# Kernel optimization log

Measured on AMD Instinct MI355X. Metric: run time of the kernel, lower is better.

## Reference

```python
import jax, jax.numpy as jnp
import numpy as np

B, G = 256, 24
N = B * G
D_IN, HEADS, D_HEAD = 128, 8, 64  # out_channels = in_channels//2 = 64, concat=False
EFF = HEADS * D_HEAD
EPS = 1e-5
SCALE = float(np.sqrt(D_HEAD))

def _gelu(x):
    return jax.nn.gelu(x, approximate=False)

def _pff(x, w1, b1, w2, b2):
    # PositionwiseFeedForward, dropout=0 (eval)
    return _gelu(x @ w1.T + b1) @ w2.T + b2

def _graph_norm_global(x, w, b, ms):
    # GraphNorm called without batch -> single graph over all N nodes
    mean = jnp.mean(x, axis=0, keepdims=True)
    out = x - mean * ms
    var = jnp.mean(out * out, axis=0, keepdims=True)
    return w * out / jnp.sqrt(var + EPS) + b

def _graph_norm(x, w, b, ms, batch, nseg):
    cnt = jax.ops.segment_sum(jnp.ones((x.shape[0],), x.dtype), batch, nseg)[:, None]
    mean = jax.ops.segment_sum(x, batch, nseg) / cnt
    out = x - mean[batch] * ms
    var = jax.ops.segment_sum(out * out, batch, nseg) / cnt
    return w * out / jnp.sqrt(var + EPS)[batch] + b

def _segment_softmax(logits, seg, nseg):
    m = jax.ops.segment_max(logits, seg, num_segments=nseg)
    e = jnp.exp(logits - m[seg])
    s = jax.ops.segment_sum(e, seg, num_segments=nseg)
    return e / (s[seg] + 1e-16)

def _attn_conv(x, edge_index, p):
    (nq_w, nq_b, nq_ms, wq, bq, wk, bk, wv, bv,
     no_w, no_b, no_ms, o_w1, o_b1, o_w2, o_b2) = p
    n = x.shape[0]
    xin = x
    xn = _graph_norm_global(x, nq_w, nq_b, nq_ms)
    q = (xn @ wq.T + bq).reshape(n, HEADS, D_HEAD)
    k = (xn @ wk.T + bk).reshape(n, HEADS, D_HEAD)
    v = (xn @ wv.T + bv).reshape(n, HEADS, D_HEAD)
    loops = jnp.arange(n, dtype=edge_index.dtype)  # add_self_loops appends
    src = jnp.concatenate([edge_index[0], loops])
    dst = jnp.concatenate([edge_index[1], loops])
    qk = jnp.sum(q[dst] * k[src], axis=-1) / SCALE          # [E', H]
    alpha = _segment_softmax(qk, dst, n)                     # segment softmax over dst
    aggr = jax.ops.segment_sum(v[src] * alpha[:, :, None], dst, num_segments=n)  # [N,H,Dh]
    aggr = aggr.mean(axis=1)                                 # concat=False: head mean -> [N,64]
    init = xin.reshape(n, D_IN // D_HEAD, D_HEAD).sum(axis=1)  # sum-fold 128 -> 64 residual
    h = aggr + init
    hn = _graph_norm_global(h, no_w, no_b, no_ms)
    return h + _pff(hn, o_w1, o_b1, o_w2, o_b2)


def setup_inputs() -> dict:
    key = jax.random.key(0)
    ks = jax.random.split(key, 12)
    # block-dense edges: fully connected within each set, no self loops
    a = np.arange(G)
    ii, jj = np.meshgrid(a, a, indexing='ij')
    m = ii != jj
    dst_l, src_l = ii[m], jj[m]
    offs = (np.arange(B) * G)[:, None]
    src = (src_l[None, :] + offs).reshape(-1)
    dst = (dst_l[None, :] + offs).reshape(-1)
    edge_index = jnp.asarray(np.stack([src, dst]), dtype=jnp.int64)
    batch = jnp.asarray(np.repeat(np.arange(B), G), dtype=jnp.int64)
    ptr = jnp.asarray(np.arange(B + 1) * G, dtype=jnp.int64)
    x = jax.random.normal(ks[0], (N, D_IN), jnp.float32)
    def lin(k, o, i):
        return jax.random.normal(k, (o, i), jnp.float32) * (1.0 / np.sqrt(i))
    d = dict(x=x, edge_index=edge_index, ptr=ptr, batch=batch)
    d.update(nq_w=jnp.ones((D_IN,)), nq_b=jnp.zeros((D_IN,)), nq_ms=jnp.ones((D_IN,)))
    d.update(wq=lin(ks[1], EFF, D_IN), bq=jnp.zeros((EFF,)),
             wk=lin(ks[2], EFF, D_IN), bk=jnp.zeros((EFF,)),
             wv=lin(ks[3], EFF, D_IN), bv=jnp.zeros((EFF,)))
    d.update(no_w=jnp.ones((D_HEAD,)), no_b=jnp.zeros((D_HEAD,)), no_ms=jnp.ones((D_HEAD,)))
    d.update(o_w1=lin(ks[4], D_HEAD, D_HEAD), o_b1=jnp.zeros((D_HEAD,)),
             o_w2=lin(ks[5], D_HEAD, D_HEAD), o_b2=jnp.zeros((D_HEAD,)))
    d.update(pn_w=jnp.ones((D_HEAD,)), pn_b=jnp.zeros((D_HEAD,)), pn_ms=jnp.ones((D_HEAD,)))
    d.update(p_w1=lin(ks[6], D_HEAD, D_HEAD), p_b1=jnp.zeros((D_HEAD,)),
             p_w2=lin(ks[7], 1, D_HEAD), p_b2=jnp.zeros((1,)))
    return d


def reference(x, edge_index, ptr, batch,
              nq_w, nq_b, nq_ms, wq, bq, wk, bk, wv, bv,
              no_w, no_b, no_ms, o_w1, o_b1, o_w2, o_b2,
              pn_w, pn_b, pn_ms, p_w1, p_b1, p_w2, p_b2):
    nseg = ptr.shape[0] - 1
    h = _attn_conv(x, edge_index,
                   (nq_w, nq_b, nq_ms, wq, bq, wk, bk, wv, bv,
                    no_w, no_b, no_ms, o_w1, o_b1, o_w2, o_b2))   # [N,64]
    hn = _graph_norm(h, pn_w, pn_b, pn_ms, batch, nseg)
    score = _pff(hn, p_w1, p_b1, p_w2, p_b2)                       # [N,1]
    w = _segment_softmax(score[:, 0], batch, nseg)[:, None]        # per-set softmax
    return jax.ops.segment_sum(x * w, batch, num_segments=nseg)    # [B, 128]
```

## Files before the change

### kernel.cpp

```cpp
#include <hip/hip_runtime.h>
#include <stdint.h>


#define N_NODES 6144
#define GSIZE 24
#define NGRAPH 256
#define DIN 128
#define DH 64
#define EFF 512
#define EPSN 1e-5f

typedef __attribute__((ext_vector_type(8))) __bf16 bf16x8;
typedef __attribute__((ext_vector_type(4))) float f32x4;
union U16B { uint4 u; bf16x8 v; unsigned short s[8]; };

__device__ inline float bf2f(unsigned short u){ return __uint_as_float(((unsigned)u)<<16); }
__device__ inline unsigned short f2bf(float f){
  unsigned u = __float_as_uint(f);
  u += 0x7fff + ((u>>16)&1);
  return (unsigned short)(u>>16);
}
__device__ inline float gelu_exact(float x){ return 0.5f*x*(1.0f+erff(x*0.70710678118654752f)); }

#define XP    0
#define HP    49152
#define WT1   81920
#define WT2   86016
#define PWT1  90112
#define FBo   94208
#define AC    94720
#define AC2   94976
#define WCVT_BYTE  385024
#define HCOMB_BYTE 778240
#define QKV_BYTE   2359296

__global__ __launch_bounds__(256)
void k_pre(const float* __restrict__ x,
           const float* __restrict__ o_w1, const float* __restrict__ o_w2,
           const float* __restrict__ p_w1,
           const float* __restrict__ o_b1, const float* __restrict__ o_b2,
           const float* __restrict__ p_b1, const float* __restrict__ p_w2,
           const float* __restrict__ p_b2,
           const float* __restrict__ wq, const float* __restrict__ wk,
           const float* __restrict__ wv,
           float* __restrict__ wsf){
  int t = threadIdx.x;
  int bi = blockIdx.x;
  if(bi < 192){
    int c = t & 127, h = t >> 7;
    float s = 0.f, q = 0.f;
    #pragma unroll
    for(int r = 0; r < 16; ++r){
      float v = x[(size_t)(bi*32 + h + 2*r)*DIN + c];
      s += v; q += v*v;
    }
    __shared__ float sm[256], sm2[256];
    sm[t] = s; sm2[t] = q;
    __syncthreads();
    if(t < 128){
      wsf[XP + bi*256 + t]       = sm[t] + sm[t+128];
      wsf[XP + bi*256 + 128 + t] = sm2[t] + sm2[t+128];
    }
    return;
  }
  if(bi < 195){
    const float* src; float* dst;
    if(bi == 192){ src = o_w1; dst = wsf + WT1; }
    else if(bi == 193){ src = o_w2; dst = wsf + WT2; }
    else { src = p_w1; dst = wsf + PWT1; }
    for(int p = t; p < DH*DH; p += 256){
      int r = p >> 6, c = p & 63;
      dst[c*DH + r] = src[p];
    }
    if(bi == 192){
      float* fb = wsf + FBo;
      if(t < 64){
        fb[t]       = o_b1[t];
        fb[64 + t]  = o_b2[t];
        fb[128 + t] = p_b1[t];
        fb[192 + t] = p_w2[t];
      }
      if(t == 0) fb[256] = p_b2[0];
    }
    return;
  }
  int j = bi - 195;
  int mat = j >> 2, seg = j & 3;
  const float* src = (mat==0) ? wq : (mat==1) ? wk : wv;
  unsigned short* dst = (unsigned short*)((char*)wsf + WCVT_BYTE)
                        + (size_t)mat*EFF*DIN + seg*16384;
  const float* sp = src + seg*16384;
  for(int e = t*8; e < 16384; e += 2048){
    float4 a = *(const float4*)(sp + e);
    float4 b = *(const float4*)(sp + e + 4);
    U16B o;
    o.s[0]=f2bf(a.x); o.s[1]=f2bf(a.y); o.s[2]=f2bf(a.z); o.s[3]=f2bf(a.w);
    o.s[4]=f2bf(b.x); o.s[5]=f2bf(b.y); o.s[6]=f2bf(b.z); o.s[7]=f2bf(b.w);
    *(uint4*)(dst + e) = o.u;
  }
}

__global__ __launch_bounds__(512)
void k_stats(const float* __restrict__ nq_w, const float* __restrict__ nq_b,
             const float* __restrict__ nq_ms, float* __restrict__ ws){
  __shared__ float redA[512], redB[512];
  int t = threadIdx.x;
  int c = t & 127, grp = t >> 7;
  float s = 0.f, q = 0.f;
  for(int p = grp*48; p < grp*48 + 48; ++p){
    s += ws[XP + p*256 + c];
    q += ws[XP + p*256 + 128 + c];
  }
  redA[t] = s; redB[t] = q;
  __syncthreads();
  if(t < 128){
    float s1 = redA[t] + redA[t+128] + redA[t+256] + redA[t+384];
    float q1 = redB[t] + redB[t+128] + redB[t+256] + redB[t+384];
    float mean = s1 * (1.0f / N_NODES);
    float ex2  = q1 * (1.0f / N_NODES);
    float cm   = mean * nq_ms[t];
    float var  = ex2 - 2.f*cm*mean + cm*cm;
    float rstd = rsqrtf(var + EPSN);
    float a    = nq_w[t] * rstd;
    ws[AC + t]       = a;
    ws[AC + 128 + t] = nq_b[t] - a*cm;
  }
}

__global__ __launch_bounds__(256)
void k_qkv(const float* __restrict__ x,
           const float* __restrict__ bq, const float* __restrict__ bk,
           const float* __restrict__ bv,
           const float* __restrict__ ws, float* __restrict__ qkv){
  __shared__ __align__(16) char lds[65536];
  char* Alds = lds;
  char* Blds = lds + 32768;
  int t = threadIdx.x;
  int mt = blockIdx.x / 12, nt = blockIdx.x % 12;
  int mat = nt >> 2, obase = (nt & 3) * 128;
  const float* A1c = ws + AC;
  const unsigned short* wsrc = (const unsigned short*)((const char*)ws + WCVT_BYTE)
                               + (size_t)mat*EFF*DIN + (size_t)obase*DIN;
  {
    int kf = (t & 31) * 4;
    float4 a4 = *(const float4*)(A1c + kf);
    float4 c4 = *(const float4*)(A1c + 128 + kf);
    #pragma unroll
    for(int it = 0; it < 16; ++it){
      int row = it*8 + (t >> 5);
      float4 v = *(const float4*)(x + (size_t)(mt*128 + row)*DIN + kf);
      ushort4 us;
      us.x = f2bf(v.x*a4.x + c4.x);
      us.y = f2bf(v.y*a4.y + c4.y);
      us.z = f2bf(v.z*a4.z + c4.z);
      us.w = f2bf(v.w*a4.w + c4.w);
      *(ushort4*)(Alds + ((row*256 + kf*2) ^ ((row & 7) << 4))) = us;
    }
  }
  {
    int kb = (t & 15) * 16;
    #pragma unroll
    for(int it = 0; it < 8; ++it){
      int row = it*16 + (t >> 4);
      uint4 w = *(const uint4*)((const char*)wsrc + row*256 + kb);
      *(uint4*)(Blds + ((row*256 + kb) ^ ((row & 7) << 4))) = w;
    }
  }
  __syncthreads();
  int wv4 = t >> 6, l = t & 63;
  int wr = wv4 >> 1, wc = wv4 & 1;
  int lm = l & 15, lq = l >> 4;
  f32x4 acc[4][4];
  #pragma unroll
  for(int m = 0; m < 4; ++m)
    #pragma unroll
    for(int n = 0; n < 4; ++n) acc[m][n] = (f32x4){0.f,0.f,0.f,0.f};
  #pragma unroll
  for(int kk = 0; kk < 4; ++kk){
    int kbyte = kk*64 + lq*16;
    bf16x8 af[4], bf[4];
    #pragma unroll
    for(int m = 0; m < 4; ++m){
      int row = wr*64 + m*16 + lm;
      af[m] = *(const bf16x8*)(Alds + ((row*256 + kbyte) ^ ((row & 7) << 4)));
    }
    #pragma unroll
    for(int n = 0; n < 4; ++n){
      int row = wc*64 + n*16 + lm;
      bf[n] = *(const bf16x8*)(Blds + ((row*256 + kbyte) ^ ((row & 7) << 4)));
    }
    #pragma unroll
    for(int m = 0; m < 4; ++m)
      #pragma unroll
      for(int n = 0; n < 4; ++n)
        acc[m][n] = __builtin_amdgcn_mfma_f32_16x16x32_bf16(af[m], bf[n], acc[m][n], 0, 0, 0);
  }
  const float* bias = (mat==0) ? bq : (mat==1) ? bk : bv;
  #pragma unroll
  for(int n = 0; n < 4; ++n){
    float bn = bias[obase + wc*64 + n*16 + lm];
    int gcol = nt*128 + wc*64 + n*16 + lm;
    #pragma unroll
    for(int m = 0; m < 4; ++m){
      int grow0 = mt*128 + wr*64 + m*16 + lq*4;
      #pragma unroll
      for(int r = 0; r < 4; ++r)
        qkv[(size_t)(grow0 + r)*1536 + gcol] = acc[m][n][r] + bn;
    }
  }
}

__global__ __launch_bounds__(512)
void k_attn(const float* __restrict__ x, const float* __restrict__ qkv,
            float* __restrict__ ws, float* __restrict__ hcomb){
  __shared__ __align__(16) float ST[8][GSIZE][28];
  __shared__ __align__(16) float hv[GSIZE][68];
  int t = threadIdx.x, g = blockIdx.x, base = g * GSIZE;
  int h = t >> 6, l = t & 63;

  for(int i = t; i < GSIZE*68; i += 512) ((float*)hv)[i] = 0.f;

  int r0 = 3*(l >> 3), j0 = 3*(l & 7);
  const float* qp = qkv + (size_t)(base + r0)*1536 + h*64;
  const float* kp = qkv + (size_t)(base + j0)*1536 + 512 + h*64;
  float s00=0.f,s01=0.f,s02=0.f,s10=0.f,s11=0.f,s12=0.f,s20=0.f,s21=0.f,s22=0.f;
  #pragma unroll
  for(int d4 = 0; d4 < 16; ++d4){
    float4 q0 = *(const float4*)(qp + d4*4);
    float4 q1 = *(const float4*)(qp + 1536 + d4*4);
    float4 q2 = *(const float4*)(qp + 3072 + d4*4);
    float4 k0 = *(const float4*)(kp + d4*4);
    float4 k1 = *(const float4*)(kp + 1536 + d4*4);
    float4 k2 = *(const float4*)(kp + 3072 + d4*4);
    s00 += q0.x*k0.x + q0.y*k0.y + q0.z*k0.z + q0.w*k0.w;
    s01 += q0.x*k1.x + q0.y*k1.y + q0.z*k1.z + q0.w*k1.w;
    s02 += q0.x*k2.x + q0.y*k2.y + q0.z*k2.z + q0.w*k2.w;
    s10 += q1.x*k0.x + q1.y*k0.y + q1.z*k0.z + q1.w*k0.w;
    s11 += q1.x*k1.x + q1.y*k1.y + q1.z*k1.z + q1.w*k1.w;
    s12 += q1.x*k2.x + q1.y*k2.y + q1.z*k2.z + q1.w*k2.w;
    s20 += q2.x*k0.x + q2.y*k0.y + q2.z*k0.z + q2.w*k0.w;
    s21 += q2.x*k1.x + q2.y*k1.y + q2.z*k1.z + q2.w*k1.w;
    s22 += q2.x*k2.x + q2.y*k2.y + q2.z*k2.z + q2.w*k2.w;
  }
  {
    float a0, a1, a2, m0, su, inv;
    a0 = s00*0.125f; a1 = s01*0.125f; a2 = s02*0.125f;
    m0 = fmaxf(fmaxf(a0, a1), a2);
    #pragma unroll
    for(int o = 1; o < 8; o <<= 1) m0 = fmaxf(m0, __shfl_xor(m0, o, 8));
    a0 = __expf(a0-m0); a1 = __expf(a1-m0); a2 = __expf(a2-m0);
    su = a0 + a1 + a2;
    #pragma unroll
    for(int o = 1; o < 8; o <<= 1) su += __shfl_xor(su, o, 8);
    inv = 1.0f/(su + 1e-16f);
    ST[h][j0+0][r0+0] = a0*inv; ST[h][j0+1][r0+0] = a1*inv; ST[h][j0+2][r0+0] = a2*inv;
    a0 = s10*0.125f; a1 = s11*0.125f; a2 = s12*0.125f;
    m0 = fmaxf(fmaxf(a0, a1), a2);
    #pragma unroll
    for(int o = 1; o < 8; o <<= 1) m0 = fmaxf(m0, __shfl_xor(m0, o, 8));
    a0 = __expf(a0-m0); a1 = __expf(a1-m0); a2 = __expf(a2-m0);
    su = a0 + a1 + a2;
    #pragma unroll
    for(int o = 1; o < 8; o <<= 1) su += __shfl_xor(su, o, 8);
    inv = 1.0f/(su + 1e-16f);
    ST[h][j0+0][r0+1] = a0*inv; ST[h][j0+1][r0+1] = a1*inv; ST[h][j0+2][r0+1] = a2*inv;
    a0 = s20*0.125f; a1 = s21*0.125f; a2 = s22*0.125f;
    m0 = fmaxf(fmaxf(a0, a1), a2);
    #pragma unroll
    for(int o = 1; o < 8; o <<= 1) m0 = fmaxf(m0, __shfl_xor(m0, o, 8));
    a0 = __expf(a0-m0); a1 = __expf(a1-m0); a2 = __expf(a2-m0);
    su = a0 + a1 + a2;
    #pragma unroll
    for(int o = 1; o < 8; o <<= 1) su += __shfl_xor(su, o, 8);
    inv = 1.0f/(su + 1e-16f);
    ST[h][j0+0][r0+2] = a0*inv; ST[h][j0+1][r0+2] = a1*inv; ST[h][j0+2][r0+2] = a2*inv;
  }
  __syncthreads();

  {
    float o24[GSIZE];
    #pragma unroll
    for(int r = 0; r < GSIZE; ++r) o24[r] = 0.f;
    const float* vp = qkv + (size_t)base*1536 + 1024 + h*64 + l;
    #pragma unroll
    for(int j = 0; j < GSIZE; ++j){
      float v = vp[(size_t)j*1536];
      #pragma unroll
      for(int rq = 0; rq < 6; ++rq){
        float4 p4 = *(const float4*)&ST[h][j][rq*4];
        o24[rq*4+0] = fmaf(p4.x, v, o24[rq*4+0]);
        o24[rq*4+1] = fmaf(p4.y, v, o24[rq*4+1]);
        o24[rq*4+2] = fmaf(p4.z, v, o24[rq*4+2]);
        o24[rq*4+3] = fmaf(p4.w, v, o24[rq*4+3]);
      }
    }
    #pragma unroll
    for(int r = 0; r < GSIZE; ++r) atomicAdd(&hv[r][l], o24[r]);
  }
  __syncthreads();

  #pragma unroll
  for(int sl = 0; sl < 3; ++sl){
    int idx = t + sl*512;
    int r = idx >> 6, d = idx & 63;
    const float* xr = x + (size_t)(base + r)*DIN;
    float hval = hv[r][d]*0.125f + xr[d] + xr[64 + d];
    hcomb[(size_t)(base + r)*DH + d] = hval;
    hv[r][d] = hval;
  }
  __syncthreads();
  if(t < 64){
    float s1 = 0.f, s2 = 0.f;
    #pragma unroll
    for(int i = 0; i < GSIZE; ++i){ float v = hv[i][t]; s1 += v; s2 += v*v; }
    ws[HP + g*128 + t]      = s1;
    ws[HP + g*128 + 64 + t] = s2;
  }
}

__global__ __launch_bounds__(256)
void k_hstats(const float* __restrict__ no_w, const float* __restrict__ no_b,
              const float* __restrict__ no_ms, float* __restrict__ ws){
  __shared__ float redA[256], redB[256];
  int t = threadIdx.x;
  int c = t & 63, grp = t >> 6;
  float s1 = 0.f, s2 = 0.f;
  for(int p = grp; p < NGRAPH; p += 4){
    s1 += ws[HP + p*128 + c];
    s2 += ws[HP + p*128 + 64 + c];
  }
  redA[t] = s1; redB[t] = s2;
  __syncthreads();
  if(t < DH){
    float a1 = redA[t] + redA[t+64] + redA[t+128] + redA[t+192];
    float a2 = redB[t] + redB[t+64] + redB[t+128] + redB[t+192];
    float mean = a1 * (1.0f / N_NODES);
    float ex2  = a2 * (1.0f / N_NODES);
    float cm   = mean * no_ms[t];
    float var  = ex2 - 2.f*cm*mean + cm*cm;
    float rstd = rsqrtf(var + EPSN);
    float a    = no_w[t] * rstd;
    ws[AC2 + t]      = a;
    ws[AC2 + 64 + t] = no_b[t] - a*cm;
  }
}

__global__ __launch_bounds__(256)
void k_final(const float* __restrict__ x,
             const float* __restrict__ hbuf, const float* __restrict__ ws,
             const float* __restrict__ pn_w, const float* __restrict__ pn_b,
             const float* __restrict__ pn_ms,
             float* __restrict__ out){
  __shared__ __align__(16) float W1[4096];
  __shared__ __align__(16) float W2[4096];
  __shared__ __align__(16) float PW1[4096];
  __shared__ __align__(16) float fbs[260];
  __shared__ __align__(16) float hs[GSIZE][68];
  __shared__ __align__(16) float hn[GSIZE][68];
  __shared__ __align__(16) float ts[GSIZE][68];
  __shared__ float a3[DH], c3[DH];
  __shared__ float scores[GSIZE], wsm[GSIZE];

  int t = threadIdx.x;
  int base = blockIdx.x * GSIZE;
  int c = t & 63, i0 = t >> 6;

  {
    const float4* s1 = (const float4*)(ws + WT1);
    const float4* s2 = (const float4*)(ws + WT2);
    const float4* s3 = (const float4*)(ws + PWT1);
    #pragma unroll
    for(int it = 0; it < 4; ++it){
      int i = t + it*256;
      ((float4*)W1)[i]  = s1[i];
      ((float4*)W2)[i]  = s2[i];
      ((float4*)PW1)[i] = s3[i];
    }
    if(t < 257) fbs[t] = ws[FBo + t];
  }
  {
    float a2 = ws[AC2 + c];
    float c2 = ws[AC2 + 64 + c];
    #pragma unroll
    for(int r = 0; r < 6; ++r){
      int i = i0 + 4*r;
      float hvv = hbuf[(size_t)(base + i)*DH + c];
      hs[i][c] = hvv;
      hn[i][c] = a2*hvv + c2;
    }
  }
  __syncthreads();

  {
    float acc[6];
    #pragma unroll
    for(int r = 0; r < 6; ++r) acc[r] = fbs[c];
    #pragma unroll 16
    for(int k = 0; k < DH; ++k){
      float w = W1[k*DH + c];
      #pragma unroll
      for(int r = 0; r < 6; ++r) acc[r] = fmaf(hn[i0 + 4*r][k], w, acc[r]);
    }
    #pragma unroll
    for(int r = 0; r < 6; ++r) ts[i0 + 4*r][c] = gelu_exact(acc[r]);
  }
  __syncthreads();

  {
    float acc[6];
    #pragma unroll
    for(int r = 0; r < 6; ++r) acc[r] = fbs[64 + c];
    #pragma unroll 16
    for(int k = 0; k < DH; ++k){
      float w = W2[k*DH + c];
      #pragma unroll
      for(int r = 0; r < 6; ++r) acc[r] = fmaf(ts[i0 + 4*r][k], w, acc[r]);
    }
    #pragma unroll
    for(int r = 0; r < 6; ++r) hs[i0 + 4*r][c] += acc[r];
  }
  __syncthreads();

  if(t < DH){
    float s1 = 0.f, s2 = 0.f;
    #pragma unroll
    for(int i = 0; i < GSIZE; i++){ float v = hs[i][t]; s1 += v; s2 += v*v; }
    float mean = s1 * (1.0f / GSIZE);
    float ex2  = s2 * (1.0f / GSIZE);
    float cm   = mean * pn_ms[t];
    float var  = ex2 - 2.f*cm*mean + cm*cm;
    float rstd = rsqrtf(var + EPSN);
    float a    = pn_w[t] * rstd;
    a3[t] = a; c3[t] = pn_b[t] - a*cm;
  }
  __syncthreads();

  {
    float acc[6];
    #pragma unroll
    for(int r = 0; r < 6; ++r) acc[r] = fbs[128 + c];
    #pragma unroll 16
    for(int k = 0; k < DH; ++k){
      float w  = PW1[k*DH + c];
      float ak = a3[k], ck = c3[k];
      #pragma unroll
      for(int r = 0; r < 6; ++r){
        float hnv = fmaf(ak, hs[i0 + 4*r][k], ck);
        acc[r] = fmaf(hnv, w, acc[r]);
      }
    }
    #pragma unroll
    for(int r = 0; r < 6; ++r) ts[i0 + 4*r][c] = gelu_exact(acc[r]);
  }
  __syncthreads();

  if(t < GSIZE){
    const float4* tp = (const float4*)ts[t];
    const float4* wp = (const float4*)(fbs + 192);
    float s = fbs[256];
    #pragma unroll
    for(int q = 0; q < 16; ++q){
      float4 a = tp[q], b = wp[q];
      s += a.x*b.x + a.y*b.y + a.z*b.z + a.w*b.w;
    }
    scores[t] = s;
  }
  __syncthreads();
  if(t < GSIZE){
    float mx = -1e30f;
    #pragma unroll
    for(int j = 0; j < GSIZE; j++) mx = fmaxf(mx, scores[j]);
    float sum = 0.f;
    #pragma unroll
    for(int j = 0; j < GSIZE; j++) sum += __expf(scores[j] - mx);
    wsm[t] = __expf(scores[t] - mx) / (sum + 1e-16f);
  }
  __syncthreads();
  if(t < DIN){
    float s = 0.f;
    #pragma unroll 8
    for(int i = 0; i < GSIZE; i++) s += wsm[i] * x[(size_t)(base+i)*DIN + t];
    out[(size_t)blockIdx.x*DIN + t] = s;
  }
}

extern "C" void kernel_launch(void* const* d_in, const int* in_sizes, int n_in,
                              void* d_out, int out_size, void* d_ws, size_t ws_size,
                              hipStream_t stream){
  (void)in_sizes; (void)n_in; (void)out_size; (void)ws_size;
  const float* x    = (const float*)d_in[0];
  const float* nq_w = (const float*)d_in[4];
  const float* nq_b = (const float*)d_in[5];
  const float* nq_ms= (const float*)d_in[6];
  const float* wq   = (const float*)d_in[7];
  const float* bq   = (const float*)d_in[8];
  const float* wk   = (const float*)d_in[9];
  const float* bk   = (const float*)d_in[10];
  const float* wv   = (const float*)d_in[11];
  const float* bv   = (const float*)d_in[12];
  const float* no_w = (const float*)d_in[13];
  const float* no_b = (const float*)d_in[14];
  const float* no_ms= (const float*)d_in[15];
  const float* o_w1 = (const float*)d_in[16];
  const float* o_b1 = (const float*)d_in[17];
  const float* o_w2 = (const float*)d_in[18];
  const float* o_b2 = (const float*)d_in[19];
  const float* pn_w = (const float*)d_in[20];
  const float* pn_b = (const float*)d_in[21];
  const float* pn_ms= (const float*)d_in[22];
  const float* p_w1 = (const float*)d_in[23];
  const float* p_b1 = (const float*)d_in[24];
  const float* p_w2 = (const float*)d_in[25];
  const float* p_b2 = (const float*)d_in[26];

  float* ws    = (float*)d_ws;
  float* hcomb = (float*)((char*)d_ws + HCOMB_BYTE);
  float* qkvb  = (float*)((char*)d_ws + QKV_BYTE);

  k_pre<<<207, 256, 0, stream>>>(x, o_w1, o_w2, p_w1, o_b1, o_b2, p_b1, p_w2, p_b2,
                                 wq, wk, wv, ws);
  k_stats<<<1, 512, 0, stream>>>(nq_w, nq_b, nq_ms, ws);
  k_qkv<<<576, 256, 0, stream>>>(x, bq, bk, bv, ws, qkvb);
  k_attn<<<NGRAPH, 512, 0, stream>>>(x, qkvb, ws, hcomb);
  k_hstats<<<1, 256, 0, stream>>>(no_w, no_b, no_ms, ws);
  k_final<<<NGRAPH, 256, 0, stream>>>(x, hcomb, ws, pn_w, pn_b, pn_ms, (float*)d_out);
}
```

Measured before the change: 195.6 us.

## Fuse global stats, QKV projection and attention into one per-graph kernel

The single-block stats kernels are folded into the consumers: every attention block recomputes the global norm stats, and k_final recomputes the output-norm stats. The QKV GEMM now runs per graph inside the attention kernel, with results kept in LDS instead of a global qkv buffer. This cuts three kernel launches and the round trip of a large intermediate through global memory. In exchange, each block redundantly reduces the global partial sums and uses a large LDS footprint (about 150KB), which lowers occupancy. MFMA tiles are also partly wasted because 24 rows are padded to 32.

```diff
diff --git a/kernel.cpp b/kernel.cpp
--- a/kernel.cpp
+++ b/kernel.cpp
@@ -14,7 +14,6 @@
 typedef __attribute__((ext_vector_type(4))) float f32x4;
 union U16B { uint4 u; bf16x8 v; unsigned short s[8]; };
 
-__device__ inline float bf2f(unsigned short u){ return __uint_as_float(((unsigned)u)<<16); }
 __device__ inline unsigned short f2bf(float f){
   unsigned u = __float_as_uint(f);
   u += 0x7fff + ((u>>16)&1);
@@ -28,11 +27,10 @@
 #define WT2   86016
 #define PWT1  90112
 #define FBo   94208
-#define AC    94720
-#define AC2   94976
 #define WCVT_BYTE  385024
 #define HCOMB_BYTE 778240
-#define QKV_BYTE   2359296
+
+#define QSTRIDE 516
 
 __global__ __launch_bounds__(256)
 void k_pre(const float* __restrict__ x,
@@ -101,149 +99,123 @@
 }
 
 __global__ __launch_bounds__(512)
-void k_stats(const float* __restrict__ nq_w, const float* __restrict__ nq_b,
-             const float* __restrict__ nq_ms, float* __restrict__ ws){
-  __shared__ float redA[512], redB[512];
-  int t = threadIdx.x;
-  int c = t & 127, grp = t >> 7;
-  float s = 0.f, q = 0.f;
-  for(int p = grp*48; p < grp*48 + 48; ++p){
-    s += ws[XP + p*256 + c];
-    q += ws[XP + p*256 + 128 + c];
-  }
-  redA[t] = s; redB[t] = q;
-  __syncthreads();
-  if(t < 128){
-    float s1 = redA[t] + redA[t+128] + redA[t+256] + redA[t+384];
-    float q1 = redB[t] + redB[t+128] + redB[t+256] + redB[t+384];
-    float mean = s1 * (1.0f / N_NODES);
-    float ex2  = q1 * (1.0f / N_NODES);
-    float cm   = mean * nq_ms[t];
-    float var  = ex2 - 2.f*cm*mean + cm*cm;
-    float rstd = rsqrtf(var + EPSN);
-    float a    = nq_w[t] * rstd;
-    ws[AC + t]       = a;
-    ws[AC + 128 + t] = nq_b[t] - a*cm;
-  }
-}
-
-__global__ __launch_bounds__(256)
-void k_qkv(const float* __restrict__ x,
-           const float* __restrict__ bq, const float* __restrict__ bk,
-           const float* __restrict__ bv,
-           const float* __restrict__ ws, float* __restrict__ qkv){
-  __shared__ __align__(16) char lds[65536];
-  char* Alds = lds;
-  char* Blds = lds + 32768;
-  int t = threadIdx.x;
-  int mt = blockIdx.x / 12, nt = blockIdx.x % 12;
-  int mat = nt >> 2, obase = (nt & 3) * 128;
-  const float* A1c = ws + AC;
-  const unsigned short* wsrc = (const unsigned short*)((const char*)ws + WCVT_BYTE)
-                               + (size_t)mat*EFF*DIN + (size_t)obase*DIN;
-  {
-    int kf = (t & 31) * 4;
-    float4 a4 = *(const float4*)(A1c + kf);
-    float4 c4 = *(const float4*)(A1c + 128 + kf);
-    #pragma unroll
-    for(int it = 0; it < 16; ++it){
-      int row = it*8 + (t >> 5);
-      float4 v = *(const float4*)(x + (size_t)(mt*128 + row)*DIN + kf);
-      ushort4 us;
-      us.x = f2bf(v.x*a4.x + c4.x);
-      us.y = f2bf(v.y*a4.y + c4.y);
-      us.z = f2bf(v.z*a4.z + c4.z);
-      us.w = f2bf(v.w*a4.w + c4.w);
-      *(ushort4*)(Alds + ((row*256 + kf*2) ^ ((row & 7) << 4))) = us;
-    }
-  }
-  {
-    int kb = (t & 15) * 16;
-    #pragma unroll
-    for(int it = 0; it < 8; ++it){
-      int row = it*16 + (t >> 4);
-      uint4 w = *(const uint4*)((const char*)wsrc + row*256 + kb);
-      *(uint4*)(Blds + ((row*256 + kb) ^ ((row & 7) << 4))) = w;
-    }
-  }
-  __syncthreads();
-  int wv4 = t >> 6, l = t & 63;
-  int wr = wv4 >> 1, wc = wv4 & 1;
-  int lm = l & 15, lq = l >> 4;
-  f32x4 acc[4][4];
+void k_attn2(const float* __restrict__ x,
+             const float* __restrict__ bq, const float* __restrict__ bk,
+             const float* __restrict__ bv,
+             const float* __restrict__ nq_w, const float* __restrict__ nq_b,
+             const float* __restrict__ nq_ms,
+             float* __restrict__ ws, float* __restrict__ hcomb){
+  __shared__ __align__(16) float qlds[3*GSIZE*QSTRIDE];
+  __shared__ __align__(16) float hv[GSIZE][68];
+  __shared__ float A1s[DIN], C1s[DIN];
+
+  int t = threadIdx.x, g = blockIdx.x, base = g*GSIZE;
+  int h = t >> 6, l = t & 63;
+  const unsigned short* wcvt = (const unsigned short*)((const char*)ws + WCVT_BYTE);
+
+  for(int i = t; i < GSIZE*68; i += 512) ((float*)hv)[i] = 0.f;
+
+  {
+    float* redA = qlds;
+    float* redB = qlds + 512;
+    int c = t & 127, grp = t >> 7;
+    float s = 0.f, q = 0.f;
+    for(int p = grp*48; p < grp*48 + 48; ++p){
+      s += ws[XP + p*256 + c];
+      q += ws[XP + p*256 + 128 + c];
+    }
+    redA[t] = s; redB[t] = q;
+    __syncthreads();
+    if(t < 128){
+      float s1 = redA[t] + redA[t+128] + redA[t+256] + redA[t+384];
+      float q1 = redB[t] + redB[t+128] + redB[t+256] + redB[t+384];
+      float mean = s1 * (1.0f / N_NODES);
+      float ex2  = q1 * (1.0f / N_NODES);
+      float cm   = mean * nq_ms[t];
+      float var  = ex2 - 2.f*cm*mean + cm*cm;
+      float rstd = rsqrtf(var + EPSN);
+      float a    = nq_w[t] * rstd;
+      A1s[t] = a; C1s[t] = nq_b[t] - a*cm;
+    }
+    __syncthreads();
+  }
+
+  int m = l & 15, lq = l >> 4;
+
+  bf16x8 afr[2][4];
   #pragma unroll
-  for(int m = 0; m < 4; ++m)
-    #pragma unroll
-    for(int n = 0; n < 4; ++n) acc[m][n] = (f32x4){0.f,0.f,0.f,0.f};
+  for(int mt = 0; mt < 2; ++mt){
+    int row = mt*16 + m; if(row > GSIZE-1) row = GSIZE-1;
+    const float* xr = x + (size_t)(base + row)*DIN;
+    #pragma unroll
+    for(int kk = 0; kk < 4; ++kk){
+      int k0 = kk*32 + lq*8;
+      float4 a = *(const float4*)(xr + k0);
+      float4 b = *(const float4*)(xr + k0 + 4);
+      U16B u;
+      u.s[0] = f2bf(a.x*A1s[k0+0] + C1s[k0+0]);
+      u.s[1] = f2bf(a.y*A1s[k0+1] + C1s[k0+1]);
+      u.s[2] = f2bf(a.z*A1s[k0+2] + C1s[k0+2]);
+      u.s[3] = f2bf(a.w*A1s[k0+3] + C1s[k0+3]);
+      u.s[4] = f2bf(b.x*A1s[k0+4] + C1s[k0+4]);
+      u.s[5] = f2bf(b.y*A1s[k0+5] + C1s[k0+5]);
+      u.s[6] = f2bf(b.z*A1s[k0+6] + C1s[k0+6]);
+      u.s[7] = f2bf(b.w*A1s[k0+7] + C1s[k0+7]);
+      afr[mt][kk] = u.v;
+    }
+  }
+
   #pragma unroll
-  for(int kk = 0; kk < 4; ++kk){
-    int kbyte = kk*64 + lq*16;
-    bf16x8 af[4], bf[4];
-    #pragma unroll
-    for(int m = 0; m < 4; ++m){
-      int row = wr*64 + m*16 + lm;
-      af[m] = *(const bf16x8*)(Alds + ((row*256 + kbyte) ^ ((row & 7) << 4)));
-    }
-    #pragma unroll
-    for(int n = 0; n < 4; ++n){
-      int row = wc*64 + n*16 + lm;
-      bf[n] = *(const bf16x8*)(Blds + ((row*256 + kbyte) ^ ((row & 7) << 4)));
-    }
-    #pragma unroll
-    for(int m = 0; m < 4; ++m)
-      #pragma unroll
-      for(int n = 0; n < 4; ++n)
-        acc[m][n] = __builtin_amdgcn_mfma_f32_16x16x32_bf16(af[m], bf[n], acc[m][n], 0, 0, 0);
-  }
-  const float* bias = (mat==0) ? bq : (mat==1) ? bk : bv;
-  #pragma unroll
-  for(int n = 0; n < 4; ++n){
-    float bn = bias[obase + wc*64 + n*16 + lm];
-    int gcol = nt*128 + wc*64 + n*16 + lm;
-    #pragma unroll
-    for(int m = 0; m < 4; ++m){
-      int grow0 = mt*128 + wr*64 + m*16 + lq*4;
-      #pragma unroll
-      for(int r = 0; r < 4; ++r)
-        qkv[(size_t)(grow0 + r)*1536 + gcol] = acc[m][n][r] + bn;
-    }
-  }
-}
-
-__global__ __launch_bounds__(512)
-void k_attn(const float* __restrict__ x, const float* __restrict__ qkv,
-            float* __restrict__ ws, float* __restrict__ hcomb){
-  __shared__ __align__(16) float ST[8][GSIZE][28];
-  __shared__ __align__(16) float hv[GSIZE][68];
-  int t = threadIdx.x, g = blockIdx.x, base = g * GSIZE;
-  int h = t >> 6, l = t & 63;
-
-  for(int i = t; i < GSIZE*68; i += 512) ((float*)hv)[i] = 0.f;
-
-  int r0 = 3*(l >> 3), j0 = 3*(l & 7);
-  const float* qp = qkv + (size_t)(base + r0)*1536 + h*64;
-  const float* kp = qkv + (size_t)(base + j0)*1536 + 512 + h*64;
-  float s00=0.f,s01=0.f,s02=0.f,s10=0.f,s11=0.f,s12=0.f,s20=0.f,s21=0.f,s22=0.f;
-  #pragma unroll
-  for(int d4 = 0; d4 < 16; ++d4){
-    float4 q0 = *(const float4*)(qp + d4*4);
-    float4 q1 = *(const float4*)(qp + 1536 + d4*4);
-    float4 q2 = *(const float4*)(qp + 3072 + d4*4);
-    float4 k0 = *(const float4*)(kp + d4*4);
-    float4 k1 = *(const float4*)(kp + 1536 + d4*4);
-    float4 k2 = *(const float4*)(kp + 3072 + d4*4);
-    s00 += q0.x*k0.x + q0.y*k0.y + q0.z*k0.z + q0.w*k0.w;
-    s01 += q0.x*k1.x + q0.y*k1.y + q0.z*k1.z + q0.w*k1.w;
-    s02 += q0.x*k2.x + q0.y*k2.y + q0.z*k2.z + q0.w*k2.w;
-    s10 += q1.x*k0.x + q1.y*k0.y + q1.z*k0.z + q1.w*k0.w;
-    s11 += q1.x*k1.x + q1.y*k1.y + q1.z*k1.z + q1.w*k1.w;
-    s12 += q1.x*k2.x + q1.y*k2.y + q1.z*k2.z + q1.w*k2.w;
-    s20 += q2.x*k0.x + q2.y*k0.y + q2.z*k0.z + q2.w*k0.w;
-    s21 += q2.x*k1.x + q2.y*k1.y + q2.z*k1.z + q2.w*k1.w;
-    s22 += q2.x*k2.x + q2.y*k2.y + q2.z*k2.z + q2.w*k2.w;
-  }
-  {
+  for(int nt = 0; nt < 12; ++nt){
+    int mat = nt >> 2, sub = nt & 3;
+    const unsigned short* wp = wcvt + (size_t)mat*EFF*DIN
+                             + (size_t)(h*64 + sub*16 + m)*DIN + lq*8;
+    const float* bias = (mat==0) ? bq : (mat==1) ? bk : bv;
+    float4 bb = *(const float4*)(bias + h*64 + sub*16 + lq*4);
+    f32x4 acc0 = {0.f,0.f,0.f,0.f}, acc1 = {0.f,0.f,0.f,0.f};
+    #pragma unroll
+    for(int kk = 0; kk < 4; ++kk){
+      U16B w8; w8.u = *(const uint4*)(wp + kk*32);
+      acc0 = __builtin_amdgcn_mfma_f32_16x16x32_bf16(w8.v, afr[0][kk], acc0, 0, 0, 0);
+      acc1 = __builtin_amdgcn_mfma_f32_16x16x32_bf16(w8.v, afr[1][kk], acc1, 0, 0, 0);
+    }
+    float* dst = qlds + mat*(GSIZE*QSTRIDE);
+    int col = h*64 + sub*16 + lq*4;
+    {
+      float4 o; o.x = acc0[0]+bb.x; o.y = acc0[1]+bb.y; o.z = acc0[2]+bb.z; o.w = acc0[3]+bb.w;
+      *(float4*)(dst + m*QSTRIDE + col) = o;
+    }
+    if(m < 8){
+      float4 o; o.x = acc1[0]+bb.x; o.y = acc1[1]+bb.y; o.z = acc1[2]+bb.z; o.w = acc1[3]+bb.w;
+      *(float4*)(dst + (16+m)*QSTRIDE + col) = o;
+    }
+  }
+
+  {
+    int r0 = 3*(l >> 3), j0 = 3*(l & 7);
+    const float* qp = qlds + r0*QSTRIDE + h*64;
+    const float* kp = qlds + GSIZE*QSTRIDE + j0*QSTRIDE + h*64;
+    float s00=0.f,s01=0.f,s02=0.f,s10=0.f,s11=0.f,s12=0.f,s20=0.f,s21=0.f,s22=0.f;
+    #pragma unroll
+    for(int d4 = 0; d4 < 16; ++d4){
+      float4 q0 = *(const float4*)(qp + d4*4);
+      float4 q1 = *(const float4*)(qp + QSTRIDE + d4*4);
+      float4 q2 = *(const float4*)(qp + 2*QSTRIDE + d4*4);
+      float4 k0 = *(const float4*)(kp + d4*4);
+      float4 k1 = *(const float4*)(kp + QSTRIDE + d4*4);
+      float4 k2 = *(const float4*)(kp + 2*QSTRIDE + d4*4);
+      s00 += q0.x*k0.x + q0.y*k0.y + q0.z*k0.z + q0.w*k0.w;
+      s01 += q0.x*k1.x + q0.y*k1.y + q0.z*k1.z + q0.w*k1.w;
+      s02 += q0.x*k2.x + q0.y*k2.y + q0.z*k2.z + q0.w*k2.w;
+      s10 += q1.x*k0.x + q1.y*k0.y + q1.z*k0.z + q1.w*k0.w;
+      s11 += q1.x*k1.x + q1.y*k1.y + q1.z*k1.z + q1.w*k1.w;
+      s12 += q1.x*k2.x + q1.y*k2.y + q1.z*k2.z + q1.w*k2.w;
+      s20 += q2.x*k0.x + q2.y*k0.y + q2.z*k0.z + q2.w*k0.w;
+      s21 += q2.x*k1.x + q2.y*k1.y + q2.z*k1.z + q2.w*k1.w;
+      s22 += q2.x*k2.x + q2.y*k2.y + q2.z*k2.z + q2.w*k2.w;
+    }
     float a0, a1, a2, m0, su, inv;
+    float* STb = qlds + h*64;
     a0 = s00*0.125f; a1 = s01*0.125f; a2 = s02*0.125f;
     m0 = fmaxf(fmaxf(a0, a1), a2);
     #pragma unroll
@@ -253,7 +225,7 @@
     #pragma unroll
     for(int o = 1; o < 8; o <<= 1) su += __shfl_xor(su, o, 8);
     inv = 1.0f/(su + 1e-16f);
-    ST[h][j0+0][r0+0] = a0*inv; ST[h][j0+1][r0+0] = a1*inv; ST[h][j0+2][r0+0] = a2*inv;
+    STb[(j0+0)*QSTRIDE + r0] = a0*inv; STb[(j0+1)*QSTRIDE + r0] = a1*inv; STb[(j0+2)*QSTRIDE + r0] = a2*inv;
     a0 = s10*0.125f; a1 = s11*0.125f; a2 = s12*0.125f;
     m0 = fmaxf(fmaxf(a0, a1), a2);
     #pragma unroll
@@ -263,7 +235,7 @@
     #pragma unroll
     for(int o = 1; o < 8; o <<= 1) su += __shfl_xor(su, o, 8);
     inv = 1.0f/(su + 1e-16f);
-    ST[h][j0+0][r0+1] = a0*inv; ST[h][j0+1][r0+1] = a1*inv; ST[h][j0+2][r0+1] = a2*inv;
+    STb[(j0+0)*QSTRIDE + r0+1] = a0*inv; STb[(j0+1)*QSTRIDE + r0+1] = a1*inv; STb[(j0+2)*QSTRIDE + r0+1] = a2*inv;
     a0 = s20*0.125f; a1 = s21*0.125f; a2 = s22*0.125f;
     m0 = fmaxf(fmaxf(a0, a1), a2);
     #pragma unroll
@@ -273,21 +245,21 @@
     #pragma unroll
     for(int o = 1; o < 8; o <<= 1) su += __shfl_xor(su, o, 8);
     inv = 1.0f/(su + 1e-16f);
-    ST[h][j0+0][r0+2] = a0*inv; ST[h][j0+1][r0+2] = a1*inv; ST[h][j0+2][r0+2] = a2*inv;
-  }
-  __syncthreads();
+    STb[(j0+0)*QSTRIDE + r0+2] = a0*inv; STb[(j0+1)*QSTRIDE + r0+2] = a1*inv; STb[(j0+2)*QSTRIDE + r0+2] = a2*inv;
+  }
 
   {
     float o24[GSIZE];
     #pragma unroll
     for(int r = 0; r < GSIZE; ++r) o24[r] = 0.f;
-    const float* vp = qkv + (size_t)base*1536 + 1024 + h*64 + l;
+    const float* vp  = qlds + 2*GSIZE*QSTRIDE + h*64 + l;
+    const float* STb = qlds + h*64;
     #pragma unroll
     for(int j = 0; j < GSIZE; ++j){
-      float v = vp[(size_t)j*1536];
+      float v = vp[j*QSTRIDE];
       #pragma unroll
       for(int rq = 0; rq < 6; ++rq){
-        float4 p4 = *(const float4*)&ST[h][j][rq*4];
+        float4 p4 = *(const float4*)(STb + j*QSTRIDE + rq*4);
         o24[rq*4+0] = fmaf(p4.x, v, o24[rq*4+0]);
         o24[rq*4+1] = fmaf(p4.y, v, o24[rq*4+1]);
         o24[rq*4+2] = fmaf(p4.z, v, o24[rq*4+2]);
@@ -319,35 +291,10 @@
 }
 
 __global__ __launch_bounds__(256)
-void k_hstats(const float* __restrict__ no_w, const float* __restrict__ no_b,
-              const float* __restrict__ no_ms, float* __restrict__ ws){
-  __shared__ float redA[256], redB[256];
-  int t = threadIdx.x;
-  int c = t & 63, grp = t >> 6;
-  float s1 = 0.f, s2 = 0.f;
-  for(int p = grp; p < NGRAPH; p += 4){
-    s1 += ws[HP + p*128 + c];
-    s2 += ws[HP + p*128 + 64 + c];
-  }
-  redA[t] = s1; redB[t] = s2;
-  __syncthreads();
-  if(t < DH){
-    float a1 = redA[t] + redA[t+64] + redA[t+128] + redA[t+192];
-    float a2 = redB[t] + redB[t+64] + redB[t+128] + redB[t+192];
-    float mean = a1 * (1.0f / N_NODES);
-    float ex2  = a2 * (1.0f / N_NODES);
-    float cm   = mean * no_ms[t];
-    float var  = ex2 - 2.f*cm*mean + cm*cm;
-    float rstd = rsqrtf(var + EPSN);
-    float a    = no_w[t] * rstd;
-    ws[AC2 + t]      = a;
-    ws[AC2 + 64 + t] = no_b[t] - a*cm;
-  }
-}
-
-__global__ __launch_bounds__(256)
 void k_final(const float* __restrict__ x,
              const float* __restrict__ hbuf, const float* __restrict__ ws,
+             const float* __restrict__ no_w, const float* __restrict__ no_b,
+             const float* __restrict__ no_ms,
              const float* __restrict__ pn_w, const float* __restrict__ pn_b,
              const float* __restrict__ pn_ms,
              float* __restrict__ out){
@@ -358,8 +305,10 @@
   __shared__ __align__(16) float hs[GSIZE][68];
   __shared__ __align__(16) float hn[GSIZE][68];
   __shared__ __align__(16) float ts[GSIZE][68];
+  __shared__ float A2s[DH], C2s[DH];
   __shared__ float a3[DH], c3[DH];
   __shared__ float scores[GSIZE], wsm[GSIZE];
+  __shared__ float redA[256], redB[256];
 
   int t = threadIdx.x;
   int base = blockIdx.x * GSIZE;
@@ -377,10 +326,30 @@
       ((float4*)PW1)[i] = s3[i];
     }
     if(t < 257) fbs[t] = ws[FBo + t];
-  }
-  {
-    float a2 = ws[AC2 + c];
-    float c2 = ws[AC2 + 64 + c];
+    int cc = t & 63, grp = t >> 6;
+    float s1r = 0.f, s2r = 0.f;
+    for(int p = grp; p < NGRAPH; p += 4){
+      s1r += ws[HP + p*128 + cc];
+      s2r += ws[HP + p*128 + 64 + cc];
+    }
+    redA[t] = s1r; redB[t] = s2r;
+  }
+  __syncthreads();
+  if(t < DH){
+    float a1 = redA[t] + redA[t+64] + redA[t+128] + redA[t+192];
+    float a2 = redB[t] + redB[t+64] + redB[t+128] + redB[t+192];
+    float mean = a1 * (1.0f / N_NODES);
+    float ex2  = a2 * (1.0f / N_NODES);
+    float cm   = mean * no_ms[t];
+    float var  = ex2 - 2.f*cm*mean + cm*cm;
+    float rstd = rsqrtf(var + EPSN);
+    float a    = no_w[t] * rstd;
+    A2s[t] = a; C2s[t] = no_b[t] - a*cm;
+  }
+  __syncthreads();
+  {
+    float a2 = A2s[c];
+    float c2 = C2s[c];
     #pragma unroll
     for(int r = 0; r < 6; ++r){
       int i = i0 + 4*r;
@@ -515,13 +484,10 @@
 
   float* ws    = (float*)d_ws;
   float* hcomb = (float*)((char*)d_ws + HCOMB_BYTE);
-  float* qkvb  = (float*)((char*)d_ws + QKV_BYTE);
 
   k_pre<<<207, 256, 0, stream>>>(x, o_w1, o_w2, p_w1, o_b1, o_b2, p_b1, p_w2, p_b2,
                                  wq, wk, wv, ws);
-  k_stats<<<1, 512, 0, stream>>>(nq_w, nq_b, nq_ms, ws);
-  k_qkv<<<576, 256, 0, stream>>>(x, bq, bk, bv, ws, qkvb);
-  k_attn<<<NGRAPH, 512, 0, stream>>>(x, qkvb, ws, hcomb);
-  k_hstats<<<1, 256, 0, stream>>>(no_w, no_b, no_ms, ws);
-  k_final<<<NGRAPH, 256, 0, stream>>>(x, hcomb, ws, pn_w, pn_b, pn_ms, (float*)d_out);
+  k_attn2<<<NGRAPH, 512, 0, stream>>>(x, bq, bk, bv, nq_w, nq_b, nq_ms, ws, hcomb);
+  k_final<<<NGRAPH, 256, 0, stream>>>(x, hcomb, ws, no_w, no_b, no_ms,
+                                      pn_w, pn_b, pn_ms, (float*)d_out);
 }
```

Measured after the change: 181.0 us. 1.08x faster.
